# Optimization experiments

Hardware: AMD Instinct MI355X
Metric: run time of the kernel (lower is better)

Reference implementation:

```python
import jax, jax.numpy as jnp
import numpy as np

G = 4          # moe_groups
EPG = 4        # experts per group = e_num // moe_groups
E = 16         # e_num
KG = 2         # moe_max_groups
K = 2          # moe_max_k
GTP = 0.9      # moe_group_top_p
TP = 0.9       # moe_top_p
SCALE = 1.0 / float(np.sqrt(G))  # group_scale


def setup_inputs() -> dict:
    key = jax.random.key(0)
    ks = jax.random.split(key, 6)
    B, T, D, H = 2, 1024, 512, 2048  # H = 4*emb_dim per SwiGLU_FFN(emb_dim, 4*emb_dim)
    x = jax.random.normal(ks[0], (B, T, D), jnp.float32)
    Wr = jax.random.normal(ks[1], (D, G), jnp.float32) * 0.02      # group_router weight
    br = jnp.zeros((G,), jnp.float32)                               # group_router bias
    Wgate = jax.random.normal(ks[2], (G, D, EPG), jnp.float32) * 0.02  # per-group gates
    bgate = jnp.zeros((G, EPG), jnp.float32)
    W1 = jax.random.normal(ks[3], (E, D, H), jnp.float32) * 0.02   # SwiGLU gate proj
    W3 = jax.random.normal(ks[4], (E, D, H), jnp.float32) * 0.02   # SwiGLU up proj
    W2 = jax.random.normal(ks[5], (E, H, D), jnp.float32) * 0.02   # SwiGLU down proj
    return {"x": x, "Wr": Wr, "br": br, "Wgate": Wgate, "bgate": bgate,
            "W1": W1, "W3": W3, "W2": W2}


def _routing_weights(xf, Wr, br, Wgate, bgate):
    # Returns combined per-(token, expert) weight (N, E): group_renorm * expert_renorm * SCALE.
    N = xf.shape[0]
    # ---- group-level top-p routing ----
    gp = jax.nn.softmax(xf @ Wr + br, axis=-1)                      # (N, G)
    order = jnp.argsort(-gp, axis=-1)
    sp_k = jnp.take_along_axis(gp, order, axis=-1)[:, :KG]          # top-KG probs, descending
    idx_k = order[:, :KG]
    act = jnp.cumsum(sp_k, axis=-1) <= GTP
    act = act.at[:, 0].set(True)                                    # always keep best group
    mp = sp_k * act
    rn = mp / (jnp.sum(mp, axis=-1, keepdims=True) + 1e-9)
    w_group = jnp.zeros((N, G), xf.dtype).at[jnp.arange(N)[:, None], idx_k].set(rn)
    # ---- expert-level top-p routing within each group ----
    ep = jax.nn.softmax(jnp.einsum('nd,gde->nge', xf, Wgate) + bgate, axis=-1)  # (N, G, EPG)
    eorder = jnp.argsort(-ep, axis=-1)
    esp = jnp.take_along_axis(ep, eorder, axis=-1)[:, :, :K]
    eidx = eorder[:, :, :K]
    eact = jnp.cumsum(esp, axis=-1) <= TP
    eact = eact.at[:, :, 0].set(True)                               # always keep best expert
    emp = esp * eact
    ern = emp / (jnp.sum(emp, axis=-1, keepdims=True) + 1e-9)
    w_exp = jnp.zeros((N, G, EPG), xf.dtype).at[
        jnp.arange(N)[:, None, None], jnp.arange(G)[None, :, None], eidx].set(ern)
    return (w_group[:, :, None] * w_exp * SCALE).reshape(N, E)      # (N, E)


def reference(x, Wr, br, Wgate, bgate, W1, W3, W2):
    B, T, D = x.shape
    xf = x.reshape(-1, D)                                           # (N, D)
    tw = _routing_weights(xf, Wr, br, Wgate, bgate)                 # (N, E)
    out = jnp.zeros_like(xf)
    for e in range(E):  # fixed structural loop over experts
        h = jax.nn.silu(xf @ W1[e]) * (xf @ W3[e])                  # SwiGLU hidden (N, H)
        out = out + tw[:, e:e + 1] * (h @ W2[e])
    return out.reshape(B, T, D)
```

## Files before the change

### kernel.cpp

```cpp
#include <hip/hip_runtime.h>
#include <math.h>

typedef unsigned short u16;
typedef unsigned int   u32;
typedef short s16x8 __attribute__((ext_vector_type(8)));
typedef float f32x4 __attribute__((ext_vector_type(4)));

#define N_TOK 2048
#define DIM   512
#define HID   2048
#define NE    16
#define NG    4
#define EPG   4
#define MAXT  2048

#define BM 64
#define BN 128
#define BK 64

#define WS_CNT    0
#define WS_OFF    128
#define WS_TOKIDX 256
#define WS_TW     (WS_TOKIDX + NE*MAXT*4)
#define WS_XB     (WS_TW + N_TOK*NE*4)
#define WS_HBUF   (WS_XB + (size_t)N_TOK*DIM*2)
#define WS_W1T    (WS_HBUF + (size_t)8192*HID*2)
#define WS_W3T    (WS_W1T + (size_t)NE*HID*DIM*2)
#define WS_W2T    (WS_W3T + (size_t)NE*HID*DIM*2)
#define WS_NEED_FAST (WS_W2T + (size_t)NE*DIM*HID*2)

__device__ __forceinline__ int* ws_i32(void* ws, size_t off) { return (int*)((char*)ws + off); }

__device__ __forceinline__ u16 f2b(float f) {
    union { float f; u32 i; } v; v.f = f;
    u32 b = v.i;
    u32 r = b + 0x7FFFu + ((b >> 16) & 1u);
    return (u16)(r >> 16);
}

__global__ __launch_bounds__(64) void routing_kernel(
    const float* __restrict__ x, const float* __restrict__ Wr, const float* __restrict__ br,
    const float* __restrict__ Wgate, const float* __restrict__ bgate, void* ws)
{
    int t = blockIdx.x;
    int lane = threadIdx.x;

    float xl[8];
    {
        const float4* xr = (const float4*)(x + (size_t)t*DIM + lane*8);
        float4 a = xr[0], b = xr[1];
        xl[0]=a.x; xl[1]=a.y; xl[2]=a.z; xl[3]=a.w;
        xl[4]=b.x; xl[5]=b.y; xl[6]=b.z; xl[7]=b.w;
    }

    {
        union { u16 h[8]; uint4 q; } pk;
        #pragma unroll
        for (int i = 0; i < 8; i++) pk.h[i] = f2b(xl[i]);
        u16* xb = (u16*)((char*)ws + WS_XB);
        *(uint4*)(xb + (size_t)t*DIM + lane*8) = pk.q;
    }

    float gl[NG] = {0.f,0.f,0.f,0.f};
    float el[NE];
    #pragma unroll
    for (int e = 0; e < NE; e++) el[e] = 0.f;

    {
        const float4* Wr4 = (const float4*)Wr;
        #pragma unroll
        for (int c = 0; c < 8; c++) {
            float4 w = Wr4[lane*8 + c];
            gl[0] += xl[c]*w.x; gl[1] += xl[c]*w.y;
            gl[2] += xl[c]*w.z; gl[3] += xl[c]*w.w;
        }
    }
    {
        const float4* Wg4 = (const float4*)Wgate;
        #pragma unroll
        for (int g = 0; g < NG; g++) {
            #pragma unroll
            for (int c = 0; c < 8; c++) {
                float4 w = Wg4[(size_t)g*DIM + lane*8 + c];
                el[g*4+0] += xl[c]*w.x; el[g*4+1] += xl[c]*w.y;
                el[g*4+2] += xl[c]*w.z; el[g*4+3] += xl[c]*w.w;
            }
        }
    }

    #pragma unroll
    for (int g = 0; g < NG; g++)
        #pragma unroll
        for (int s = 32; s; s >>= 1) gl[g] += __shfl_xor(gl[g], s);
    #pragma unroll
    for (int e = 0; e < NE; e++)
        #pragma unroll
        for (int s = 32; s; s >>= 1) el[e] += __shfl_xor(el[e], s);

    if (lane != 0) return;

    float gp[NG];
    float mx = -1e30f;
    #pragma unroll
    for (int g = 0; g < NG; g++) { gl[g] += br[g]; mx = fmaxf(mx, gl[g]); }
    float sum = 0.f;
    #pragma unroll
    for (int g = 0; g < NG; g++) { gp[g] = expf(gl[g] - mx); sum += gp[g]; }
    #pragma unroll
    for (int g = 0; g < NG; g++) gp[g] /= sum;

    int i0 = 0;
    #pragma unroll
    for (int g = 1; g < NG; g++) if (gp[g] > gp[i0]) i0 = g;
    int i1 = -1;
    #pragma unroll
    for (int g = 0; g < NG; g++) { if (g == i0) continue; if (i1 < 0 || gp[g] > gp[i1]) i1 = g; }

    bool act1 = (gp[i0] + gp[i1]) <= 0.9f;
    float mp0 = gp[i0], mp1 = act1 ? gp[i1] : 0.f;
    float inv = 1.f / (mp0 + mp1 + 1e-9f);
    float wg[NG] = {0.f,0.f,0.f,0.f};
    wg[i0] = mp0 * inv;
    wg[i1] = mp1 * inv;

    float tw[NE];
    #pragma unroll
    for (int g = 0; g < NG; g++) {
        float ep[EPG];
        float emx = -1e30f;
        #pragma unroll
        for (int j = 0; j < EPG; j++) {
            float v = el[g*4 + j] + bgate[g*4 + j];
            ep[j] = v; emx = fmaxf(emx, v);
        }
        float es = 0.f;
        #pragma unroll
        for (int j = 0; j < EPG; j++) { ep[j] = expf(ep[j] - emx); es += ep[j]; }
        #pragma unroll
        for (int j = 0; j < EPG; j++) ep[j] /= es;

        int j0 = 0;
        #pragma unroll
        for (int j = 1; j < EPG; j++) if (ep[j] > ep[j0]) j0 = j;
        int j1 = -1;
        #pragma unroll
        for (int j = 0; j < EPG; j++) { if (j == j0) continue; if (j1 < 0 || ep[j] > ep[j1]) j1 = j; }

        bool ea1 = (ep[j0] + ep[j1]) <= 0.9f;
        float e0 = ep[j0], e1 = ea1 ? ep[j1] : 0.f;
        float einv = 1.f / (e0 + e1 + 1e-9f);
        float we[EPG] = {0.f,0.f,0.f,0.f};
        we[j0] = e0 * einv;
        we[j1] = e1 * einv;
        #pragma unroll
        for (int j = 0; j < EPG; j++) tw[g*4 + j] = wg[g] * we[j] * 0.5f;
    }

    float* twT = (float*)((char*)ws + WS_TW);
    #pragma unroll
    for (int e = 0; e < NE; e++) twT[(size_t)e*N_TOK + t] = tw[e];
}

__global__ __launch_bounds__(64) void expert_lists_kernel(void* ws)
{
    int e = blockIdx.x;
    int lane = threadIdx.x;
    const float* twT = (const float*)((char*)ws + WS_TW) + (size_t)e*N_TOK;
    int* tok = ws_i32(ws, WS_TOKIDX) + e*MAXT;
    int* cnt = ws_i32(ws, WS_CNT);

    float v[32];
    #pragma unroll
    for (int r = 0; r < 32; r++) v[r] = twT[r*64 + lane];

    unsigned long long lanemask = (1ull << lane) - 1ull;
    int base = 0;
    #pragma unroll
    for (int r = 0; r < 32; r++) {
        bool a = v[r] > 0.f;
        unsigned long long m = __ballot(a);
        int pre = __popcll(m & lanemask);
        if (a) tok[base + pre] = r*64 + lane;
        base += __popcll(m);
    }
    if (lane == 0) cnt[e] = base;
}

__global__ void scan_kernel(void* ws)
{
    if (threadIdx.x == 0) {
        int* cnt = ws_i32(ws, WS_CNT);
        int* off = ws_i32(ws, WS_OFF);
        int s = 0;
        for (int e = 0; e < NE; e++) { off[e] = s; s += cnt[e]; }
        off[NE] = s;
    }
}

__global__ __launch_bounds__(256) void transpose_all_kernel(
    const float* __restrict__ W1, const float* __restrict__ W3,
    const float* __restrict__ W2, void* ws)
{
    int z = blockIdx.z;
    int mat = z >> 4, e = z & 15;
    const float* src; u16* dst; int K, N, k0, n0;
    if (mat == 0)      { src = W1; dst = (u16*)((char*)ws + WS_W1T); K = DIM; N = HID; n0 = blockIdx.x*64; k0 = blockIdx.y*64; }
    else if (mat == 1) { src = W3; dst = (u16*)((char*)ws + WS_W3T); K = DIM; N = HID; n0 = blockIdx.x*64; k0 = blockIdx.y*64; }
    else               { src = W2; dst = (u16*)((char*)ws + WS_W2T); K = HID; N = DIM; k0 = blockIdx.x*64; n0 = blockIdx.y*64; }

    const float* s = src + (size_t)e*K*N;
    u16* d = dst + (size_t)e*N*K;

    __shared__ u16 T[64*72];
    int tid = threadIdx.x;

    #pragma unroll
    for (int it = 0; it < 4; it++) {
        int idx = tid + it*256;
        int kr = idx >> 4, nc = (idx & 15) * 4;
        float4 v = *(const float4*)(s + (size_t)(k0+kr)*N + n0 + nc);
        T[(nc+0)*72 + kr] = f2b(v.x);
        T[(nc+1)*72 + kr] = f2b(v.y);
        T[(nc+2)*72 + kr] = f2b(v.z);
        T[(nc+3)*72 + kr] = f2b(v.w);
    }
    __syncthreads();
    #pragma unroll
    for (int it = 0; it < 2; it++) {
        int idx = tid + it*256;
        int nr = idx >> 3, sg = idx & 7;
        *(s16x8*)(d + (size_t)(n0+nr)*K + k0 + sg*8) = *(const s16x8*)(&T[nr*72 + sg*8]);
    }
}

__global__ __launch_bounds__(256) void gemm1_fast(void* ws)
{
    int e  = blockIdx.z;
    const int* cnt = ws_i32(ws, WS_CNT);
    int ce = cnt[e];
    int m0 = blockIdx.y * BM;
    if (m0 >= ce) return;
    int n0 = blockIdx.x * BN;

    const int* off = ws_i32(ws, WS_OFF);
    const int* tok = ws_i32(ws, WS_TOKIDX) + e*MAXT;
    const u16* xb  = (const u16*)((char*)ws + WS_XB);
    const u16* W1T = (const u16*)((char*)ws + WS_W1T) + (size_t)e*HID*DIM;
    const u16* W3T = (const u16*)((char*)ws + WS_W3T) + (size_t)e*HID*DIM;
    u16* hbuf = (u16*)((char*)ws + WS_HBUF);
    int obase = off[e] + m0;

    __shared__ u16 As[BM*BK];
    __shared__ u16 Bs0[BN*BK];
    __shared__ u16 Bs1[BN*BK];
    __shared__ int rowtok[BM];

    int tid = threadIdx.x;
    if (tid < BM) {
        int m = m0 + tid;
        rowtok[tid] = tok[m < ce ? m : (ce - 1)];
    }
    __syncthreads();

    int wave = tid >> 6, lane = tid & 63;
    int quad = lane >> 4, l16 = lane & 15;
    int swz  = l16 & 7;

    f32x4 acc1[4][2], acc3[4][2];
    #pragma unroll
    for (int mt = 0; mt < 4; mt++)
        #pragma unroll
        for (int nt = 0; nt < 2; nt++) {
            acc1[mt][nt] = (f32x4){0.f,0.f,0.f,0.f};
            acc3[mt][nt] = (f32x4){0.f,0.f,0.f,0.f};
        }

    for (int k0 = 0; k0 < DIM; k0 += BK) {
        #pragma unroll
        for (int it = 0; it < 2; it++) {
            int idx = tid + it*256;
            int r = idx >> 3, sg = idx & 7;
            *(s16x8*)(&As[r*BK + ((sg ^ (r & 7)) << 3)]) =
                *(const s16x8*)(xb + (size_t)rowtok[r]*DIM + k0 + sg*8);
        }
        #pragma unroll
        for (int it = 0; it < 4; it++) {
            int idx = tid + it*256;
            int r = idx >> 3, sg = idx & 7;
            int dst = r*BK + ((sg ^ (r & 7)) << 3);
            size_t srcoff = (size_t)(n0 + r)*DIM + k0 + sg*8;
            *(s16x8*)(&Bs0[dst]) = *(const s16x8*)(W1T + srcoff);
            *(s16x8*)(&Bs1[dst]) = *(const s16x8*)(W3T + srcoff);
        }
        __syncthreads();

        #pragma unroll
        for (int kk = 0; kk < BK; kk += 32) {
            int jj = (kk >> 3) + quad;
            int so = ((jj ^ swz) << 3);
            s16x8 af[4];
            #pragma unroll
            for (int mt = 0; mt < 4; mt++)
                af[mt] = *(const s16x8*)(&As[(mt*16 + l16)*BK + so]);
            #pragma unroll
            for (int nt = 0; nt < 2; nt++) {
                int n = wave*32 + nt*16 + l16;
                s16x8 b1 = *(const s16x8*)(&Bs0[n*BK + so]);
                s16x8 b3 = *(const s16x8*)(&Bs1[n*BK + so]);
                #pragma unroll
                for (int mt = 0; mt < 4; mt++) {
                    acc1[mt][nt] = __builtin_amdgcn_mfma_f32_16x16x32_bf16(af[mt], b1, acc1[mt][nt], 0, 0, 0);
                    acc3[mt][nt] = __builtin_amdgcn_mfma_f32_16x16x32_bf16(af[mt], b3, acc3[mt][nt], 0, 0, 0);
                }
            }
        }
        __syncthreads();
    }

    #pragma unroll
    for (int mt = 0; mt < 4; mt++) {
        #pragma unroll
        for (int r = 0; r < 4; r++) {
            int row = mt*16 + quad*4 + r;
            if (m0 + row < ce) {
                #pragma unroll
                for (int nt = 0; nt < 2; nt++) {
                    float a = acc1[mt][nt][r];
                    float b = acc3[mt][nt][r];
                    float h = (a / (1.f + expf(-a))) * b;
                    int col = wave*32 + nt*16 + l16;
                    hbuf[(size_t)(obase + row)*HID + n0 + col] = f2b(h);
                }
            }
        }
    }
}

__global__ __launch_bounds__(256) void gemm2_fast(void* ws, float* __restrict__ out)
{
    int e  = blockIdx.z;
    const int* cnt = ws_i32(ws, WS_CNT);
    int ce = cnt[e];
    int m0 = blockIdx.y * BM;
    if (m0 >= ce) return;
    int n0 = blockIdx.x * BN;

    const int* off = ws_i32(ws, WS_OFF);
    const int* tok = ws_i32(ws, WS_TOKIDX) + e*MAXT;
    const float* twT = (const float*)((char*)ws + WS_TW);
    const u16* hbuf = (const u16*)((char*)ws + WS_HBUF);
    const u16* W2T = (const u16*)((char*)ws + WS_W2T) + (size_t)e*DIM*HID;
    int abase = off[e] + m0;
    int total = off[NE];

    __shared__ u16 As[BM*BK];
    __shared__ u16 Bs[BN*BK];

    int tid = threadIdx.x;
    int wave = tid >> 6, lane = tid & 63;
    int quad = lane >> 4, l16 = lane & 15;
    int swz  = l16 & 7;

    f32x4 acc[4][2];
    #pragma unroll
    for (int mt = 0; mt < 4; mt++)
        #pragma unroll
        for (int nt = 0; nt < 2; nt++) acc[mt][nt] = (f32x4){0.f,0.f,0.f,0.f};

    for (int k0 = 0; k0 < HID; k0 += BK) {
        #pragma unroll
        for (int it = 0; it < 2; it++) {
            int idx = tid + it*256;
            int r = idx >> 3, sg = idx & 7;
            int ar = abase + r;
            if (ar > total - 1) ar = total - 1;
            *(s16x8*)(&As[r*BK + ((sg ^ (r & 7)) << 3)]) =
                *(const s16x8*)(hbuf + (size_t)ar*HID + k0 + sg*8);
        }
        #pragma unroll
        for (int it = 0; it < 4; it++) {
            int idx = tid + it*256;
            int r = idx >> 3, sg = idx & 7;
            *(s16x8*)(&Bs[r*BK + ((sg ^ (r & 7)) << 3)]) =
                *(const s16x8*)(W2T + (size_t)(n0 + r)*HID + k0 + sg*8);
        }
        __syncthreads();

        #pragma unroll
        for (int kk = 0; kk < BK; kk += 32) {
            int jj = (kk >> 3) + quad;
            int so = ((jj ^ swz) << 3);
            s16x8 af[4];
            #pragma unroll
            for (int mt = 0; mt < 4; mt++)
                af[mt] = *(const s16x8*)(&As[(mt*16 + l16)*BK + so]);
            #pragma unroll
            for (int nt = 0; nt < 2; nt++) {
                int n = wave*32 + nt*16 + l16;
                s16x8 bfr = *(const s16x8*)(&Bs[n*BK + so]);
                #pragma unroll
                for (int mt = 0; mt < 4; mt++)
                    acc[mt][nt] = __builtin_amdgcn_mfma_f32_16x16x32_bf16(af[mt], bfr, acc[mt][nt], 0, 0, 0);
            }
        }
        __syncthreads();
    }

    #pragma unroll
    for (int mt = 0; mt < 4; mt++) {
        #pragma unroll
        for (int r = 0; r < 4; r++) {
            int row = mt*16 + quad*4 + r;
            if (m0 + row < ce) {
                int t = tok[m0 + row];
                float s = twT[(size_t)e*N_TOK + t];
                #pragma unroll
                for (int nt = 0; nt < 2; nt++) {
                    int col = wave*32 + nt*16 + l16;
                    atomicAdd(out + (size_t)t*DIM + n0 + col, acc[mt][nt][r] * s);
                }
            }
        }
    }
}

extern "C" void kernel_launch(void* const* d_in, const int* in_sizes, int n_in,
                              void* d_out, int out_size, void* d_ws, size_t ws_size,
                              hipStream_t stream)
{
    const float* x     = (const float*)d_in[0];
    const float* Wr    = (const float*)d_in[1];
    const float* br    = (const float*)d_in[2];
    const float* Wgate = (const float*)d_in[3];
    const float* bgate = (const float*)d_in[4];
    const float* W1    = (const float*)d_in[5];
    const float* W3    = (const float*)d_in[6];
    const float* W2    = (const float*)d_in[7];
    float* out = (float*)d_out;

    hipMemsetAsync(d_out, 0, (size_t)out_size*sizeof(float), stream);

    transpose_all_kernel<<<dim3(32, 8, 48), 256, 0, stream>>>(W1, W3, W2, d_ws);
    routing_kernel<<<N_TOK, 64, 0, stream>>>(x, Wr, br, Wgate, bgate, d_ws);
    expert_lists_kernel<<<NE, 64, 0, stream>>>(d_ws);
    scan_kernel<<<1, 64, 0, stream>>>(d_ws);
    gemm1_fast<<<dim3(HID/BN, N_TOK/BM, NE), 256, 0, stream>>>(d_ws);
    gemm2_fast<<<dim3(DIM/BN, N_TOK/BM, NE), 256, 0, stream>>>(d_ws, out);
}
```

Before: 375.9 us.

## Load GEMM tiles with direct global-to-LDS loads and fuse expert list scan

Both expert GEMM kernels now stage their A and B tiles with global_load_lds instructions, which write straight into shared memory and skip the register round trip. Per-lane row pointers carry the XOR swizzle, so each wave fills 8-row slices and the existing fragment reads still line up. Separately, the per-expert list building and the offset scan are merged into one 1024-thread block, removing a kernel launch. The risk is that the swizzled layout must exactly match the LDS write pattern of the direct-load instruction, and the loads remain synchronous with no double buffering.

```diff
diff --git a/kernel.cpp b/kernel.cpp
--- a/kernel.cpp
+++ b/kernel.cpp
@@ -27,7 +27,6 @@
 #define WS_W1T    (WS_HBUF + (size_t)8192*HID*2)
 #define WS_W3T    (WS_W1T + (size_t)NE*HID*DIM*2)
 #define WS_W2T    (WS_W3T + (size_t)NE*HID*DIM*2)
-#define WS_NEED_FAST (WS_W2T + (size_t)NE*DIM*HID*2)
 
 __device__ __forceinline__ int* ws_i32(void* ws, size_t off) { return (int*)((char*)ws + off); }
 
@@ -36,6 +35,11 @@
     u32 b = v.i;
     u32 r = b + 0x7FFFu + ((b >> 16) & 1u);
     return (u16)(r >> 16);
+}
+
+__device__ __forceinline__ void gl_lds16(const u16* g, u16* l) {
+    __builtin_amdgcn_global_load_lds((const __attribute__((address_space(1))) void*)g,
+                                     (__attribute__((address_space(3))) void*)l, 16, 0, 0);
 }
 
 __global__ __launch_bounds__(64) void routing_kernel(
@@ -161,13 +165,13 @@
     for (int e = 0; e < NE; e++) twT[(size_t)e*N_TOK + t] = tw[e];
 }
 
-__global__ __launch_bounds__(64) void expert_lists_kernel(void* ws)
-{
-    int e = blockIdx.x;
-    int lane = threadIdx.x;
+__global__ __launch_bounds__(1024) void expert_scan_kernel(void* ws)
+{
+    int tid = threadIdx.x;
+    int e = tid >> 6, lane = tid & 63;
     const float* twT = (const float*)((char*)ws + WS_TW) + (size_t)e*N_TOK;
     int* tok = ws_i32(ws, WS_TOKIDX) + e*MAXT;
-    int* cnt = ws_i32(ws, WS_CNT);
+    __shared__ int scnt[NE];
 
     float v[32];
     #pragma unroll
@@ -179,20 +183,16 @@
     for (int r = 0; r < 32; r++) {
         bool a = v[r] > 0.f;
         unsigned long long m = __ballot(a);
-        int pre = __popcll(m & lanemask);
-        if (a) tok[base + pre] = r*64 + lane;
+        if (a) tok[base + __popcll(m & lanemask)] = r*64 + lane;
         base += __popcll(m);
     }
-    if (lane == 0) cnt[e] = base;
-}
-
-__global__ void scan_kernel(void* ws)
-{
-    if (threadIdx.x == 0) {
+    if (lane == 0) scnt[e] = base;
+    __syncthreads();
+    if (tid == 0) {
         int* cnt = ws_i32(ws, WS_CNT);
         int* off = ws_i32(ws, WS_OFF);
         int s = 0;
-        for (int e = 0; e < NE; e++) { off[e] = s; s += cnt[e]; }
+        for (int i = 0; i < NE; i++) { cnt[i] = scnt[i]; off[i] = s; s += scnt[i]; }
         off[NE] = s;
     }
 }
@@ -265,6 +265,18 @@
     int wave = tid >> 6, lane = tid & 63;
     int quad = lane >> 4, l16 = lane & 15;
     int swz  = l16 & 7;
+    int r8 = lane >> 3, sg = lane & 7;
+    int swk = ((sg ^ r8) << 3);
+
+    const u16* arow0 = xb + (size_t)rowtok[wave*16 + r8]*DIM + swk;
+    const u16* arow1 = xb + (size_t)rowtok[wave*16 + 8 + r8]*DIM + swk;
+    const u16* b1row[4]; const u16* b3row[4];
+    #pragma unroll
+    for (int i = 0; i < 4; i++) {
+        size_t nr = (size_t)(n0 + wave*32 + i*8 + r8)*DIM + swk;
+        b1row[i] = W1T + nr;
+        b3row[i] = W3T + nr;
+    }
 
     f32x4 acc1[4][2], acc3[4][2];
     #pragma unroll
@@ -276,21 +288,12 @@
         }
 
     for (int k0 = 0; k0 < DIM; k0 += BK) {
-        #pragma unroll
-        for (int it = 0; it < 2; it++) {
-            int idx = tid + it*256;
-            int r = idx >> 3, sg = idx & 7;
-            *(s16x8*)(&As[r*BK + ((sg ^ (r & 7)) << 3)]) =
-                *(const s16x8*)(xb + (size_t)rowtok[r]*DIM + k0 + sg*8);
-        }
-        #pragma unroll
-        for (int it = 0; it < 4; it++) {
-            int idx = tid + it*256;
-            int r = idx >> 3, sg = idx & 7;
-            int dst = r*BK + ((sg ^ (r & 7)) << 3);
-            size_t srcoff = (size_t)(n0 + r)*DIM + k0 + sg*8;
-            *(s16x8*)(&Bs0[dst]) = *(const s16x8*)(W1T + srcoff);
-            *(s16x8*)(&Bs1[dst]) = *(const s16x8*)(W3T + srcoff);
+        gl_lds16(arow0 + k0, &As[(wave*16)*BK]);
+        gl_lds16(arow1 + k0, &As[(wave*16 + 8)*BK]);
+        #pragma unroll
+        for (int i = 0; i < 4; i++) {
+            gl_lds16(b1row[i] + k0, &Bs0[(wave*32 + i*8)*BK]);
+            gl_lds16(b3row[i] + k0, &Bs1[(wave*32 + i*8)*BK]);
         }
         __syncthreads();
 
@@ -360,6 +363,17 @@
     int wave = tid >> 6, lane = tid & 63;
     int quad = lane >> 4, l16 = lane & 15;
     int swz  = l16 & 7;
+    int r8 = lane >> 3, sg = lane & 7;
+    int swk = ((sg ^ r8) << 3);
+
+    int ar0 = abase + wave*16 + r8;      if (ar0 > total - 1) ar0 = total - 1;
+    int ar1 = abase + wave*16 + 8 + r8;  if (ar1 > total - 1) ar1 = total - 1;
+    const u16* arow0 = hbuf + (size_t)ar0*HID + swk;
+    const u16* arow1 = hbuf + (size_t)ar1*HID + swk;
+    const u16* brow[4];
+    #pragma unroll
+    for (int i = 0; i < 4; i++)
+        brow[i] = W2T + (size_t)(n0 + wave*32 + i*8 + r8)*HID + swk;
 
     f32x4 acc[4][2];
     #pragma unroll
@@ -368,22 +382,11 @@
         for (int nt = 0; nt < 2; nt++) acc[mt][nt] = (f32x4){0.f,0.f,0.f,0.f};
 
     for (int k0 = 0; k0 < HID; k0 += BK) {
-        #pragma unroll
-        for (int it = 0; it < 2; it++) {
-            int idx = tid + it*256;
-            int r = idx >> 3, sg = idx & 7;
-            int ar = abase + r;
-            if (ar > total - 1) ar = total - 1;
-            *(s16x8*)(&As[r*BK + ((sg ^ (r & 7)) << 3)]) =
-                *(const s16x8*)(hbuf + (size_t)ar*HID + k0 + sg*8);
-        }
-        #pragma unroll
-        for (int it = 0; it < 4; it++) {
-            int idx = tid + it*256;
-            int r = idx >> 3, sg = idx & 7;
-            *(s16x8*)(&Bs[r*BK + ((sg ^ (r & 7)) << 3)]) =
-                *(const s16x8*)(W2T + (size_t)(n0 + r)*HID + k0 + sg*8);
-        }
+        gl_lds16(arow0 + k0, &As[(wave*16)*BK]);
+        gl_lds16(arow1 + k0, &As[(wave*16 + 8)*BK]);
+        #pragma unroll
+        for (int i = 0; i < 4; i++)
+            gl_lds16(brow[i] + k0, &Bs[(wave*32 + i*8)*BK]);
         __syncthreads();
 
         #pragma unroll
@@ -442,8 +445,7 @@
 
     transpose_all_kernel<<<dim3(32, 8, 48), 256, 0, stream>>>(W1, W3, W2, d_ws);
     routing_kernel<<<N_TOK, 64, 0, stream>>>(x, Wr, br, Wgate, bgate, d_ws);
-    expert_lists_kernel<<<NE, 64, 0, stream>>>(d_ws);
-    scan_kernel<<<1, 64, 0, stream>>>(d_ws);
+    expert_scan_kernel<<<1, 1024, 0, stream>>>(d_ws);
     gemm1_fast<<<dim3(HID/BN, N_TOK/BM, NE), 256, 0, stream>>>(d_ws);
     gemm2_fast<<<dim3(DIM/BN, N_TOK/BM, NE), 256, 0, stream>>>(d_ws, out);
 }
```

New measurement: 360.6 us. 4.1% less time.
